# Performance work log

Hardware: AMD Instinct MI355X
Metric: run time of the kernel (lower is better)

The kernel has to match this reference:

```python
import jax, jax.numpy as jnp
import numpy as np

H = 8                                  # n_heads
MULS = [256, 128, 64]                  # multiplicities of attention_irreps * n_heads (l=0,1,2)
L_DIMS = [1, 3, 5]                     # 2l+1 for l = 0, 1, 2
NUM_IRREPS_PER_HEAD = sum(m // H for m in MULS)   # 32+16+8 = 56
ATTN_NORM = 1.0 / np.sqrt(NUM_IRREPS_PER_HEAD)


def _split(x):
    """Split flat irreps array [..., 960] into per-l blocks [..., mul, 2l+1]."""
    blocks, off = [], 0
    for m, d in zip(MULS, L_DIMS):
        blocks.append(x[..., off:off + m * d].reshape(x.shape[:-1] + (m, d)))
        off += m * d
    return blocks


def _e3_linear(blocks, Ws):
    # e3nn Linear: per-irrep channel mixing with 1/sqrt(fan_in) path normalization
    return [jnp.einsum('...mi,mn->...ni', b, W) / np.sqrt(b.shape[-2])
            for b, W in zip(blocks, Ws)]


def _mul_to_axis(blocks):
    # split multiplicity axis into [H, mul_per_head]
    return [b.reshape(b.shape[:-2] + (H, b.shape[-2] // H, b.shape[-1])) for b in blocks]


def _forward(x, wq0, wq1, wq2, wk0, wk1, wk2, wv0, wv1, wv2):
    xb = _split(x)
    q = _mul_to_axis(_e3_linear(xb, [wq0, wq1, wq2]))   # each [b, n, H, m, d]
    k = _mul_to_axis(_e3_linear(xb, [wk0, wk1, wk2]))
    v = _mul_to_axis(_e3_linear(xb, [wv0, wv1, wv2]))

    # elementwise tensor product filtered to 0e: per-irrep invariant dot / sqrt(2l+1),
    # then summed over all irrep channels (sum over axis=-1 in the original)
    logits = 0.0
    for qb, kb, d in zip(q, k, L_DIMS):
        logits = logits + jnp.einsum('bqhmd,bkhmd->bqkh', qb, kb) / np.sqrt(d)

    # softmax over the key-orbital axis (axis=-2 of [b, q, k, h])
    w = jax.nn.softmax(logits * ATTN_NORM, axis=2)

    # weighted sum over keys per irrep, then axis_to_mul(-2): merge head axis into mul
    outs = []
    for vb in v:
        u = jnp.einsum('bqkh,bkhmd->bqhmd', w, vb)      # [b, q, H, m, d]
        outs.append(u.reshape(u.shape[:2] + (-1,)))     # [b, q, H*m*d]
    update = jnp.concatenate(outs, axis=-1)             # [b, q, 960]

    return x + update  # residual: input irreps == update irreps


def setup_inputs() -> dict:
    key = jax.random.key(0)
    ks = jax.random.split(key, 10)
    B, N, D = 1024, 64, 960
    inp = {"x": jax.random.normal(ks[0], (B, N, D), dtype=jnp.float32)}
    names = ["wq0", "wq1", "wq2", "wk0", "wk1", "wk2", "wv0", "wv1", "wv2"]
    shapes = [(256, 256), (128, 128), (64, 64)] * 3
    for i, (nm, sh) in enumerate(zip(names, shapes)):
        inp[nm] = jax.random.normal(ks[i + 1], sh, dtype=jnp.float32)
    return inp


def reference(x, wq0, wq1, wq2, wk0, wk1, wk2, wv0, wv1, wv2):
    return _forward(x, wq0, wq1, wq2, wk0, wk1, wk2, wv0, wv1, wv2)
```

## Files before the change

### kernel.cpp

```cpp
#include <hip/hip_runtime.h>
#include <stdint.h>

typedef __attribute__((ext_vector_type(8))) short short8v;
typedef __attribute__((ext_vector_type(4))) float f32x4;

#define ATTN_NORM 0.13363062095621219f
#define LOG2E 1.4426950408889634f

__device__ __forceinline__ unsigned short f2bf(float f) {
  union { float f; uint32_t u; } v; v.f = f;
  uint32_t u = v.u;
  u += 0x7fffu + ((u >> 16) & 1u);
  return (unsigned short)(u >> 16);
}

__device__ __forceinline__ uint32_t pack2bf(float lo, float hi) {
  return (uint32_t)f2bf(lo) | ((uint32_t)f2bf(hi) << 16);
}

__global__ void prep_w2(const float* q0, const float* q1, const float* q2,
                        const float* k0, const float* k1, const float* k2,
                        const float* v0, const float* v1, const float* v2,
                        unsigned short* ws) {
  int e = blockIdx.x * 256 + threadIdx.x;
  if (e >= 258048) return;
  int b = e >> 9, idx = e & 511;
  int lane = idx >> 3, eo = idx & 7;
  int mat = b / 168, r = b - mat * 168;
  int li, n, MUL, c2, ks;
  if (r < 128) {
    li = 0; MUL = 256;
    int h = r >> 4, t = r & 15;
    int nt = t >> 3; c2 = (t >> 2) & 1; ks = t & 3;
    n = h * 32 + nt * 16 + (lane & 15);
  } else if (r < 160) {
    li = 1; MUL = 128;
    int r2 = r - 128; int h = r2 >> 2, t = r2 & 3;
    c2 = t >> 1; ks = t & 1;
    n = h * 16 + (lane & 15);
  } else {
    li = 2; MUL = 64;
    int r2 = r - 160; int hp = r2 >> 1;
    c2 = r2 & 1; ks = 0;
    n = hp * 16 + (lane & 15);
  }
  int m = c2 * (MUL >> 1) + ks * 32 + (lane >> 4) * 8 + eo;
  const float* src;
  if (mat == 0)      src = (li == 0) ? q0 : (li == 1) ? q1 : q2;
  else if (mat == 1) src = (li == 0) ? k0 : (li == 1) ? k1 : k2;
  else               src = (li == 0) ? v0 : (li == 1) ? v1 : v2;
  float scale = (li == 0) ? 0.0625f : (li == 1) ? 0.08838834764831845f : 0.125f;
  if (mat == 0) {
    float qext = (li == 0) ? 1.0f : (li == 1) ? 0.5773502691896258f : 0.4472135954999579f;
    scale *= ATTN_NORM * LOG2E * qext;
  }
  ws[e] = f2bf(src[m * MUL + n] * scale);
}

template<int W, int D, int XO, int BLK0, int NB>
__device__ __forceinline__ void conv_pass(const float* __restrict__ xp,
                                          unsigned short* __restrict__ xo,
                                          unsigned short* __restrict__ lds, int tid) {
  constexpr int PITCH = W + 8;
  #pragma unroll 2
  for (int f = tid; f < 64 * (W / 4); f += 256) {
    int tok = f / (W / 4);
    int c4 = f - tok * (W / 4);
    float4 v = *(const float4*)(xp + tok * 960 + XO + c4 * 4);
    uint2 pk = make_uint2(pack2bf(v.x, v.y), pack2bf(v.z, v.w));
    *(uint2*)(lds + tok * PITCH + c4 * 4) = pk;
  }
  __syncthreads();
  #pragma unroll 2
  for (int f = tid; f < NB * 64; f += 256) {
    int bl = f >> 6, lane = f & 63;
    int mb, i, qt;
    if (D == 1) {
      int c2 = bl >> 4, t = bl & 15;
      mb = c2 * 128 + (t >> 2) * 32; i = 0; qt = t & 3;
    } else if (D == 3) {
      int c2 = bl / 24; int t = bl - c2 * 24;
      int ks = t / 12; int rt = t - ks * 12;
      mb = c2 * 64 + ks * 32; i = rt >> 2; qt = rt & 3;
    } else {
      int c2 = bl / 20; int rt = bl - c2 * 20;
      mb = c2 * 32; i = rt >> 2; qt = rt & 3;
    }
    int tok = qt * 16 + (lane & 15);
    int m0 = mb + (lane >> 4) * 8;
    const unsigned short* base = lds + tok * PITCH + m0 * D + i;
    union { unsigned short o[8]; short8v s; } pk;
    #pragma unroll
    for (int e = 0; e < 8; ++e) pk.o[e] = base[e * D];
    *(short8v*)(xo + (BLK0 + bl) * 512 + lane * 8) = pk.s;
  }
}

__launch_bounds__(256)
__global__ void conv_x4(const float* __restrict__ x, unsigned short* __restrict__ xw) {
  __shared__ unsigned short lds[25088];
  int bid = blockIdx.x, tid = threadIdx.x;
  int b, pass;
  if (bid < 1024)       { b = bid;        pass = 0; }
  else if (bid < 2048)  { b = bid - 1024; pass = 1; }
  else                  { b = bid - 2048; pass = 2; }
  const float* xp = x + (size_t)b * 61440;
  unsigned short* xo = xw + (size_t)b * 61440;
  if (pass == 0)      conv_pass<256, 1,   0,  0, 32>(xp, xo, lds, tid);
  else if (pass == 1) conv_pass<384, 3, 256, 32, 48>(xp, xo, lds, tid);
  else                conv_pass<320, 5, 640, 80, 40>(xp, xo, lds, tid);
}

template<int L>
__device__ __forceinline__ void qkv_l(const unsigned short* __restrict__ xwb,
                                      const unsigned short* __restrict__ ws,
                                      char* __restrict__ sQ, char* __restrict__ sK,
                                      char* __restrict__ sVT,
                                      int h, int lane, int wvi) {
  constexpr int D    = (L == 0) ? 1 : (L == 1) ? 3 : 5;
  constexpr int NPL  = (L == 0) ? 32 : (L == 1) ? 16 : 8;
  constexpr int NT   = (L == 0) ? 2 : 1;
  constexpr int KS   = (L == 0) ? 4 : (L == 1) ? 2 : 1;
  constexpr int COFF = (L == 0) ? 0 : (L == 1) ? 32 : 80;
  constexpr int XB   = (L == 0) ? 0 : (L == 1) ? 32 : 80;
  constexpr int XC2  = KS * 4 * D;
  constexpr int NG   = 2 * KS;
  const int l15 = lane & 15, blk = lane >> 4;

  short8v xf[NG][D];
  #pragma unroll
  for (int g = 0; g < NG; ++g) {
    const int c2 = g / KS, ks = g - c2 * KS;
    #pragma unroll
    for (int j = 0; j < D; ++j)
      xf[g][j] = *(const short8v*)(xwb + (XB + c2 * XC2 + ks * 4 * D + j * 4 + wvi) * 512 + lane * 8);
  }

  f32x4 acc[3][NT][D];
  #pragma unroll
  for (int a = 0; a < 3; ++a)
    #pragma unroll
    for (int nt = 0; nt < NT; ++nt)
      #pragma unroll
      for (int j = 0; j < D; ++j)
        acc[a][nt][j] = (f32x4){0.f, 0.f, 0.f, 0.f};

  #pragma unroll
  for (int g = 0; g < NG; ++g) {
    const int c2 = g / KS, ks = g - c2 * KS;
    #pragma unroll
    for (int mat = 0; mat < 3; ++mat) {
      #pragma unroll
      for (int nt = 0; nt < NT; ++nt) {
        int wb;
        if constexpr (L == 0)      wb = mat * 168 + h * 16 + nt * 8 + c2 * 4 + ks;
        else if constexpr (L == 1) wb = mat * 168 + 128 + h * 4 + c2 * 2 + ks;
        else                       wb = mat * 168 + 160 + (h >> 1) * 2 + c2;
        short8v wf = *(const short8v*)(ws + wb * 512 + lane * 8);
        #pragma unroll
        for (int j = 0; j < D; ++j)
          acc[mat][nt][j] = __builtin_amdgcn_mfma_f32_16x16x32_bf16(wf, xf[g][j], acc[mat][nt][j], 0, 0, 0);
      }
    }
  }

  const int q = wvi * 16 + l15;
  const int qsw = (q & 7) << 4;
  #pragma unroll
  for (int nt = 0; nt < NT; ++nt) {
    #pragma unroll
    for (int j = 0; j < D; ++j) {
      int cb; bool valid;
      if constexpr (L == 2) { valid = ((blk >> 1) == (h & 1)); cb = COFF + j * NPL + (blk & 1) * 4; }
      else                  { valid = true;                    cb = COFF + j * NPL + nt * 16 + blk * 4; }
      if (valid) {
        uint32_t q01 = pack2bf(acc[0][nt][j][0], acc[0][nt][j][1]);
        uint32_t q23 = pack2bf(acc[0][nt][j][2], acc[0][nt][j][3]);
        uint32_t k01 = pack2bf(acc[1][nt][j][0], acc[1][nt][j][1]);
        uint32_t k23 = pack2bf(acc[1][nt][j][2], acc[1][nt][j][3]);
        int sw = (cb * 2) ^ qsw;
        *(uint2*)(sQ + q * 256 + sw) = make_uint2(q01, q23);
        *(uint2*)(sK + q * 256 + sw) = make_uint2(k01, k23);
        #pragma unroll
        for (int reg = 0; reg < 4; ++reg) {
          int c = cb + reg;
          *(unsigned short*)(sVT + c * 128 + ((q * 2) ^ ((c & 7) << 4))) = f2bf(acc[2][nt][j][reg]);
        }
      }
    }
  }
}

__launch_bounds__(256, 3)
__global__ void orbattn6(const float* __restrict__ x,
                         const unsigned short* __restrict__ ws,
                         const unsigned short* __restrict__ xw,
                         float* __restrict__ out) {
  extern __shared__ char smem[];
  char* sQ  = smem;
  char* sK  = smem + 16384;
  char* sVT = smem + 32768;
  char* sP  = smem;
  int tid = threadIdx.x;
  int bid = blockIdx.x;
  int xcd = bid & 7, t = bid >> 3;
  int h = t & 7;
  int b = (t >> 3) * 8 + xcd;
  const float* xb = x + (size_t)b * 61440;
  float* ob = out + (size_t)b * 61440;
  const unsigned short* xwb = xw + (size_t)b * 61440;
  const int lane = tid & 63, wvi = tid >> 6, l15 = lane & 15, blk = lane >> 4;

  for (int f = tid; f < 512; f += 256) {
    int q = f >> 3, c = 120 + (f & 7);
    int sw = (c * 2) ^ ((q & 7) << 4);
    *(unsigned short*)(sQ + q * 256 + sw) = 0;
    *(unsigned short*)(sK + q * 256 + sw) = 0;
    *(unsigned short*)(sVT + c * 128 + ((q * 2) ^ ((c & 7) << 4))) = 0;
  }

  qkv_l<0>(xwb, ws, sQ, sK, sVT, h, lane, wvi);
  qkv_l<1>(xwb, ws, sQ, sK, sVT, h, lane, wvi);
  qkv_l<2>(xwb, ws, sQ, sK, sVT, h, lane, wvi);
  __syncthreads();

  f32x4 lacc[4];
  #pragma unroll
  for (int kt = 0; kt < 4; ++kt) lacc[kt] = (f32x4){0.f, 0.f, 0.f, 0.f};
  #pragma unroll
  for (int ks = 0; ks < 4; ++ks) {
    int qr = wvi * 16 + l15;
    int bc = (ks * 32 + blk * 8) * 2;
    short8v qf = *(const short8v*)(sQ + qr * 256 + (bc ^ ((qr & 7) << 4)));
    #pragma unroll
    for (int kt = 0; kt < 4; ++kt) {
      int kr = kt * 16 + l15;
      short8v kf = *(const short8v*)(sK + kr * 256 + (bc ^ ((kr & 7) << 4)));
      lacc[kt] = __builtin_amdgcn_mfma_f32_16x16x32_bf16(qf, kf, lacc[kt], 0, 0, 0);
    }
  }
  float preg[4][4];
  #pragma unroll
  for (int reg = 0; reg < 4; ++reg) {
    float mx = fmaxf(fmaxf(lacc[0][reg], lacc[1][reg]), fmaxf(lacc[2][reg], lacc[3][reg]));
    #pragma unroll
    for (int dd = 1; dd <= 8; dd <<= 1) mx = fmaxf(mx, __shfl_xor(mx, dd, 64));
    float s = 0.f;
    #pragma unroll
    for (int kt = 0; kt < 4; ++kt) { preg[reg][kt] = exp2f(lacc[kt][reg] - mx); s += preg[reg][kt]; }
    #pragma unroll
    for (int dd = 1; dd <= 8; dd <<= 1) s += __shfl_xor(s, dd, 64);
    float inv = 1.0f / s;
    #pragma unroll
    for (int kt = 0; kt < 4; ++kt) preg[reg][kt] *= inv;
  }
  __syncthreads();

  #pragma unroll
  for (int reg = 0; reg < 4; ++reg) {
    int q = wvi * 16 + blk * 4 + reg;
    #pragma unroll
    for (int kt = 0; kt < 4; ++kt) {
      int k = kt * 16 + l15;
      *(unsigned short*)(sP + q * 128 + ((k * 2) ^ ((q & 7) << 4))) = f2bf(preg[reg][kt]);
    }
  }
  __syncthreads();

  f32x4 uacc[8];
  #pragma unroll
  for (int ct = 0; ct < 8; ++ct) uacc[ct] = (f32x4){0.f, 0.f, 0.f, 0.f};
  #pragma unroll
  for (int ks = 0; ks < 2; ++ks) {
    int qr = wvi * 16 + l15;
    int bc = (ks * 32 + blk * 8) * 2;
    short8v pf = *(const short8v*)(sP + qr * 128 + (bc ^ ((qr & 7) << 4)));
    #pragma unroll
    for (int ct = 0; ct < 8; ++ct) {
      int cr = ct * 16 + l15;
      short8v vf = *(const short8v*)(sVT + cr * 128 + (bc ^ ((cr & 7) << 4)));
      uacc[ct] = __builtin_amdgcn_mfma_f32_16x16x32_bf16(pf, vf, uacc[ct], 0, 0, 0);
    }
  }
  #pragma unroll
  for (int ct = 0; ct < 8; ++ct) {
    int c = ct * 16 + l15;
    if (c < 120) {
      int o;
      if (c < 32) o = h * 32 + c;
      else if (c < 80) { int cc = c - 32; int i = cc >> 4, nl = cc & 15; o = 256 + (h * 16 + nl) * 3 + i; }
      else             { int cc = c - 80; int i = cc >> 3, nl = cc & 7;  o = 640 + (h * 8 + nl) * 5 + i; }
      #pragma unroll
      for (int reg = 0; reg < 4; ++reg) {
        int q = wvi * 16 + blk * 4 + reg;
        int gi = q * 960 + o;
        ob[gi] = xb[gi] + uacc[ct][reg];
      }
    }
  }
}

extern "C" void kernel_launch(void* const* d_in, const int* in_sizes, int n_in,
                              void* d_out, int out_size, void* d_ws, size_t ws_size,
                              hipStream_t stream) {
  const float* x = (const float*)d_in[0];
  unsigned short* wsw = (unsigned short*)d_ws;
  unsigned short* xw = (unsigned short*)((char*)d_ws + 516096);
  float* out = (float*)d_out;
  prep_w2<<<1008, 256, 0, stream>>>(
      (const float*)d_in[1], (const float*)d_in[2], (const float*)d_in[3],
      (const float*)d_in[4], (const float*)d_in[5], (const float*)d_in[6],
      (const float*)d_in[7], (const float*)d_in[8], (const float*)d_in[9], wsw);
  conv_x4<<<3072, 256, 0, stream>>>(x, xw);
  hipFuncSetAttribute((const void*)orbattn6, hipFuncAttributeMaxDynamicSharedMemorySize, 49152);
  orbattn6<<<8192, 256, 49152, stream>>>(x, wsw, xw, out);
}
```

Measured before the change: 328.3 us.

## Defer V projection, reuse LDS regions, and stage output for vectorized residual stores

Splits the fused QKV projection so V is computed after softmax, writing V^T into the freed K region of LDS. This cuts shared memory from 48KB to 32KB and the live accumulators per phase, so occupancy can rise from 3 to 4 blocks per CU. The PV result is staged in LDS so the residual add and output write use contiguous float4 loads and stores instead of scattered scalar ones. In exchange the x tiles are reloaded for the V pass, and two extra barriers are added.

```diff
diff --git a/kernel.cpp b/kernel.cpp
--- a/kernel.cpp
+++ b/kernel.cpp
@@ -112,11 +112,10 @@
 }
 
 template<int L>
-__device__ __forceinline__ void qkv_l(const unsigned short* __restrict__ xwb,
-                                      const unsigned short* __restrict__ ws,
-                                      char* __restrict__ sQ, char* __restrict__ sK,
-                                      char* __restrict__ sVT,
-                                      int h, int lane, int wvi) {
+__device__ __forceinline__ void qk_l(const unsigned short* __restrict__ xwb,
+                                     const unsigned short* __restrict__ ws,
+                                     char* __restrict__ sQ, char* __restrict__ sK,
+                                     int h, int lane, int wvi) {
   constexpr int D    = (L == 0) ? 1 : (L == 1) ? 3 : 5;
   constexpr int NPL  = (L == 0) ? 32 : (L == 1) ? 16 : 8;
   constexpr int NT   = (L == 0) ? 2 : 1;
@@ -136,9 +135,9 @@
       xf[g][j] = *(const short8v*)(xwb + (XB + c2 * XC2 + ks * 4 * D + j * 4 + wvi) * 512 + lane * 8);
   }
 
-  f32x4 acc[3][NT][D];
-  #pragma unroll
-  for (int a = 0; a < 3; ++a)
+  f32x4 acc[2][NT][D];
+  #pragma unroll
+  for (int a = 0; a < 2; ++a)
     #pragma unroll
     for (int nt = 0; nt < NT; ++nt)
       #pragma unroll
@@ -149,7 +148,7 @@
   for (int g = 0; g < NG; ++g) {
     const int c2 = g / KS, ks = g - c2 * KS;
     #pragma unroll
-    for (int mat = 0; mat < 3; ++mat) {
+    for (int mat = 0; mat < 2; ++mat) {
       #pragma unroll
       for (int nt = 0; nt < NT; ++nt) {
         int wb;
@@ -181,26 +180,88 @@
         int sw = (cb * 2) ^ qsw;
         *(uint2*)(sQ + q * 256 + sw) = make_uint2(q01, q23);
         *(uint2*)(sK + q * 256 + sw) = make_uint2(k01, k23);
+      }
+    }
+  }
+}
+
+template<int L>
+__device__ __forceinline__ void v_l(const unsigned short* __restrict__ xwb,
+                                    const unsigned short* __restrict__ ws,
+                                    char* __restrict__ sVT,
+                                    int h, int lane, int wvi) {
+  constexpr int D    = (L == 0) ? 1 : (L == 1) ? 3 : 5;
+  constexpr int NPL  = (L == 0) ? 32 : (L == 1) ? 16 : 8;
+  constexpr int NT   = (L == 0) ? 2 : 1;
+  constexpr int KS   = (L == 0) ? 4 : (L == 1) ? 2 : 1;
+  constexpr int COFF = (L == 0) ? 0 : (L == 1) ? 32 : 80;
+  constexpr int XB   = (L == 0) ? 0 : (L == 1) ? 32 : 80;
+  constexpr int XC2  = KS * 4 * D;
+  constexpr int NG   = 2 * KS;
+  const int l15 = lane & 15, blk = lane >> 4;
+
+  short8v xf[NG][D];
+  #pragma unroll
+  for (int g = 0; g < NG; ++g) {
+    const int c2 = g / KS, ks = g - c2 * KS;
+    #pragma unroll
+    for (int j = 0; j < D; ++j)
+      xf[g][j] = *(const short8v*)(xwb + (XB + c2 * XC2 + ks * 4 * D + j * 4 + wvi) * 512 + lane * 8);
+  }
+
+  f32x4 acc[NT][D];
+  #pragma unroll
+  for (int nt = 0; nt < NT; ++nt)
+    #pragma unroll
+    for (int j = 0; j < D; ++j)
+      acc[nt][j] = (f32x4){0.f, 0.f, 0.f, 0.f};
+
+  #pragma unroll
+  for (int g = 0; g < NG; ++g) {
+    const int c2 = g / KS, ks = g - c2 * KS;
+    #pragma unroll
+    for (int nt = 0; nt < NT; ++nt) {
+      int wb;
+      if constexpr (L == 0)      wb = 2 * 168 + h * 16 + nt * 8 + c2 * 4 + ks;
+      else if constexpr (L == 1) wb = 2 * 168 + 128 + h * 4 + c2 * 2 + ks;
+      else                       wb = 2 * 168 + 160 + (h >> 1) * 2 + c2;
+      short8v wf = *(const short8v*)(ws + wb * 512 + lane * 8);
+      #pragma unroll
+      for (int j = 0; j < D; ++j)
+        acc[nt][j] = __builtin_amdgcn_mfma_f32_16x16x32_bf16(wf, xf[g][j], acc[nt][j], 0, 0, 0);
+    }
+  }
+
+  const int q = wvi * 16 + l15;
+  #pragma unroll
+  for (int nt = 0; nt < NT; ++nt) {
+    #pragma unroll
+    for (int j = 0; j < D; ++j) {
+      int cb; bool valid;
+      if constexpr (L == 2) { valid = ((blk >> 1) == (h & 1)); cb = COFF + j * NPL + (blk & 1) * 4; }
+      else                  { valid = true;                    cb = COFF + j * NPL + nt * 16 + blk * 4; }
+      if (valid) {
         #pragma unroll
         for (int reg = 0; reg < 4; ++reg) {
           int c = cb + reg;
-          *(unsigned short*)(sVT + c * 128 + ((q * 2) ^ ((c & 7) << 4))) = f2bf(acc[2][nt][j][reg]);
+          *(unsigned short*)(sVT + c * 128 + ((q * 2) ^ ((c & 7) << 4))) = f2bf(acc[nt][j][reg]);
         }
       }
     }
   }
 }
 
-__launch_bounds__(256, 3)
-__global__ void orbattn6(const float* __restrict__ x,
+__launch_bounds__(256, 4)
+__global__ void orbattn7(const float* __restrict__ x,
                          const unsigned short* __restrict__ ws,
                          const unsigned short* __restrict__ xw,
                          float* __restrict__ out) {
   extern __shared__ char smem[];
   char* sQ  = smem;
   char* sK  = smem + 16384;
-  char* sVT = smem + 32768;
   char* sP  = smem;
+  char* sVT = smem + 16384;
+  float* sU = (float*)smem;
   int tid = threadIdx.x;
   int bid = blockIdx.x;
   int xcd = bid & 7, t = bid >> 3;
@@ -216,12 +277,11 @@
     int sw = (c * 2) ^ ((q & 7) << 4);
     *(unsigned short*)(sQ + q * 256 + sw) = 0;
     *(unsigned short*)(sK + q * 256 + sw) = 0;
-    *(unsigned short*)(sVT + c * 128 + ((q * 2) ^ ((c & 7) << 4))) = 0;
-  }
-
-  qkv_l<0>(xwb, ws, sQ, sK, sVT, h, lane, wvi);
-  qkv_l<1>(xwb, ws, sQ, sK, sVT, h, lane, wvi);
-  qkv_l<2>(xwb, ws, sQ, sK, sVT, h, lane, wvi);
+  }
+
+  qk_l<0>(xwb, ws, sQ, sK, h, lane, wvi);
+  qk_l<1>(xwb, ws, sQ, sK, h, lane, wvi);
+  qk_l<2>(xwb, ws, sQ, sK, h, lane, wvi);
   __syncthreads();
 
   f32x4 lacc[4];
@@ -265,6 +325,13 @@
       *(unsigned short*)(sP + q * 128 + ((k * 2) ^ ((q & 7) << 4))) = f2bf(preg[reg][kt]);
     }
   }
+  for (int f = tid; f < 512; f += 256) {
+    int q = f & 63, c = 120 + (f >> 6);
+    *(unsigned short*)(sVT + c * 128 + ((q * 2) ^ ((c & 7) << 4))) = 0;
+  }
+  v_l<0>(xwb, ws, sVT, h, lane, wvi);
+  v_l<1>(xwb, ws, sVT, h, lane, wvi);
+  v_l<2>(xwb, ws, sVT, h, lane, wvi);
   __syncthreads();
 
   f32x4 uacc[8];
@@ -282,21 +349,34 @@
       uacc[ct] = __builtin_amdgcn_mfma_f32_16x16x32_bf16(pf, vf, uacc[ct], 0, 0, 0);
     }
   }
+  __syncthreads();
+
   #pragma unroll
   for (int ct = 0; ct < 8; ++ct) {
     int c = ct * 16 + l15;
     if (c < 120) {
-      int o;
-      if (c < 32) o = h * 32 + c;
-      else if (c < 80) { int cc = c - 32; int i = cc >> 4, nl = cc & 15; o = 256 + (h * 16 + nl) * 3 + i; }
-      else             { int cc = c - 80; int i = cc >> 3, nl = cc & 7;  o = 640 + (h * 8 + nl) * 5 + i; }
+      int col;
+      if (c < 32) col = c;
+      else if (c < 80) { int cc = c - 32; col = 32 + (cc & 15) * 3 + (cc >> 4); }
+      else             { int cc = c - 80; col = 80 + (cc & 7) * 5 + (cc >> 3); }
       #pragma unroll
       for (int reg = 0; reg < 4; ++reg) {
-        int q = wvi * 16 + blk * 4 + reg;
-        int gi = q * 960 + o;
-        ob[gi] = xb[gi] + uacc[ct][reg];
+        int tok = wvi * 16 + blk * 4 + reg;
+        sU[tok * 124 + col] = uacc[ct][reg];
       }
     }
+  }
+  __syncthreads();
+
+  const int hb0 = h * 32, hb1 = 256 + h * 48, hb2 = 640 + h * 40;
+  for (int f = tid; f < 1920; f += 256) {
+    int tok = f / 30;
+    int s4 = (f - tok * 30) * 4;
+    int o = (s4 < 32) ? (hb0 + s4) : (s4 < 80) ? (hb1 + s4 - 32) : (hb2 + s4 - 80);
+    f32x4 u = *(const f32x4*)(sU + tok * 124 + s4);
+    f32x4 xv = *(const f32x4*)(xb + tok * 960 + o);
+    f32x4 r = u + xv;
+    *(f32x4*)(ob + tok * 960 + o) = r;
   }
 }
 
@@ -312,6 +392,6 @@
       (const float*)d_in[4], (const float*)d_in[5], (const float*)d_in[6],
       (const float*)d_in[7], (const float*)d_in[8], (const float*)d_in[9], wsw);
   conv_x4<<<3072, 256, 0, stream>>>(x, xw);
-  hipFuncSetAttribute((const void*)orbattn6, hipFuncAttributeMaxDynamicSharedMemorySize, 49152);
-  orbattn6<<<8192, 256, 49152, stream>>>(x, wsw, xw, out);
-}
+  hipFuncSetAttribute((const void*)orbattn7, hipFuncAttributeMaxDynamicSharedMemorySize, 32768);
+  orbattn7<<<8192, 256, 32768, stream>>>(x, wsw, xw, out);
+}
```

Result: slower. 374.9 us (+14.2%).

## Keep V projection in registers and alias V^T over K buffer to cut LDS

Applied to the files above, without the earlier changes.

The V projection accumulators now stay in registers (10 f32x4 per lane) through the logits and softmax phases and are written to LDS only after K is no longer needed, so V^T reuses the K region. This cuts dynamic shared memory from 48KB to 32KB per block, and launch bounds go from 3 to 4 blocks per CU to raise occupancy. The cost is 40 extra live VGPRs across the softmax phase, which under the tighter register budget could cause spills.

```diff
diff --git a/kernel.cpp b/kernel.cpp
--- a/kernel.cpp
+++ b/kernel.cpp
@@ -115,7 +115,7 @@
 __device__ __forceinline__ void qkv_l(const unsigned short* __restrict__ xwb,
                                       const unsigned short* __restrict__ ws,
                                       char* __restrict__ sQ, char* __restrict__ sK,
-                                      char* __restrict__ sVT,
+                                      f32x4* __restrict__ vacc,
                                       int h, int lane, int wvi) {
   constexpr int D    = (L == 0) ? 1 : (L == 1) ? 3 : 5;
   constexpr int NPL  = (L == 0) ? 32 : (L == 1) ? 16 : 8;
@@ -125,6 +125,7 @@
   constexpr int XB   = (L == 0) ? 0 : (L == 1) ? 32 : 80;
   constexpr int XC2  = KS * 4 * D;
   constexpr int NG   = 2 * KS;
+  constexpr int VOFF = (L == 0) ? 0 : (L == 1) ? 2 : 5;
   const int l15 = lane & 15, blk = lane >> 4;
 
   short8v xf[NG][D];
@@ -136,9 +137,9 @@
       xf[g][j] = *(const short8v*)(xwb + (XB + c2 * XC2 + ks * 4 * D + j * 4 + wvi) * 512 + lane * 8);
   }
 
-  f32x4 acc[3][NT][D];
-  #pragma unroll
-  for (int a = 0; a < 3; ++a)
+  f32x4 acc[2][NT][D];
+  #pragma unroll
+  for (int a = 0; a < 2; ++a)
     #pragma unroll
     for (int nt = 0; nt < NT; ++nt)
       #pragma unroll
@@ -149,7 +150,7 @@
   for (int g = 0; g < NG; ++g) {
     const int c2 = g / KS, ks = g - c2 * KS;
     #pragma unroll
-    for (int mat = 0; mat < 3; ++mat) {
+    for (int mat = 0; mat < 2; ++mat) {
       #pragma unroll
       for (int nt = 0; nt < NT; ++nt) {
         int wb;
@@ -161,6 +162,17 @@
         for (int j = 0; j < D; ++j)
           acc[mat][nt][j] = __builtin_amdgcn_mfma_f32_16x16x32_bf16(wf, xf[g][j], acc[mat][nt][j], 0, 0, 0);
       }
+    }
+    #pragma unroll
+    for (int nt = 0; nt < NT; ++nt) {
+      int wb;
+      if constexpr (L == 0)      wb = 2 * 168 + h * 16 + nt * 8 + c2 * 4 + ks;
+      else if constexpr (L == 1) wb = 2 * 168 + 128 + h * 4 + c2 * 2 + ks;
+      else                       wb = 2 * 168 + 160 + (h >> 1) * 2 + c2;
+      short8v wf = *(const short8v*)(ws + wb * 512 + lane * 8);
+      #pragma unroll
+      for (int j = 0; j < D; ++j)
+        vacc[VOFF + nt * D + j] = __builtin_amdgcn_mfma_f32_16x16x32_bf16(wf, xf[g][j], vacc[VOFF + nt * D + j], 0, 0, 0);
     }
   }
 
@@ -181,26 +193,50 @@
         int sw = (cb * 2) ^ qsw;
         *(uint2*)(sQ + q * 256 + sw) = make_uint2(q01, q23);
         *(uint2*)(sK + q * 256 + sw) = make_uint2(k01, k23);
+      }
+    }
+  }
+}
+
+template<int L>
+__device__ __forceinline__ void vwrite_l(char* __restrict__ sVT,
+                                         const f32x4* __restrict__ vacc,
+                                         int h, int lane, int wvi) {
+  constexpr int D    = (L == 0) ? 1 : (L == 1) ? 3 : 5;
+  constexpr int NPL  = (L == 0) ? 32 : (L == 1) ? 16 : 8;
+  constexpr int NT   = (L == 0) ? 2 : 1;
+  constexpr int COFF = (L == 0) ? 0 : (L == 1) ? 32 : 80;
+  constexpr int VOFF = (L == 0) ? 0 : (L == 1) ? 2 : 5;
+  const int l15 = lane & 15, blk = lane >> 4;
+  const int q = wvi * 16 + l15;
+  #pragma unroll
+  for (int nt = 0; nt < NT; ++nt) {
+    #pragma unroll
+    for (int j = 0; j < D; ++j) {
+      int cb; bool valid;
+      if constexpr (L == 2) { valid = ((blk >> 1) == (h & 1)); cb = COFF + j * NPL + (blk & 1) * 4; }
+      else                  { valid = true;                    cb = COFF + j * NPL + nt * 16 + blk * 4; }
+      if (valid) {
         #pragma unroll
         for (int reg = 0; reg < 4; ++reg) {
           int c = cb + reg;
-          *(unsigned short*)(sVT + c * 128 + ((q * 2) ^ ((c & 7) << 4))) = f2bf(acc[2][nt][j][reg]);
+          *(unsigned short*)(sVT + c * 128 + ((q * 2) ^ ((c & 7) << 4))) = f2bf(vacc[VOFF + nt * D + j][reg]);
         }
       }
     }
   }
 }
 
-__launch_bounds__(256, 3)
-__global__ void orbattn6(const float* __restrict__ x,
-                         const unsigned short* __restrict__ ws,
-                         const unsigned short* __restrict__ xw,
-                         float* __restrict__ out) {
+__launch_bounds__(256, 4)
+__global__ void orbattn11(const float* __restrict__ x,
+                          const unsigned short* __restrict__ ws,
+                          const unsigned short* __restrict__ xw,
+                          float* __restrict__ out) {
   extern __shared__ char smem[];
   char* sQ  = smem;
   char* sK  = smem + 16384;
-  char* sVT = smem + 32768;
   char* sP  = smem;
+  char* sVT = smem + 16384;
   int tid = threadIdx.x;
   int bid = blockIdx.x;
   int xcd = bid & 7, t = bid >> 3;
@@ -216,12 +252,15 @@
     int sw = (c * 2) ^ ((q & 7) << 4);
     *(unsigned short*)(sQ + q * 256 + sw) = 0;
     *(unsigned short*)(sK + q * 256 + sw) = 0;
-    *(unsigned short*)(sVT + c * 128 + ((q * 2) ^ ((c & 7) << 4))) = 0;
-  }
-
-  qkv_l<0>(xwb, ws, sQ, sK, sVT, h, lane, wvi);
-  qkv_l<1>(xwb, ws, sQ, sK, sVT, h, lane, wvi);
-  qkv_l<2>(xwb, ws, sQ, sK, sVT, h, lane, wvi);
+  }
+
+  f32x4 vacc[10];
+  #pragma unroll
+  for (int i = 0; i < 10; ++i) vacc[i] = (f32x4){0.f, 0.f, 0.f, 0.f};
+
+  qkv_l<0>(xwb, ws, sQ, sK, vacc, h, lane, wvi);
+  qkv_l<1>(xwb, ws, sQ, sK, vacc, h, lane, wvi);
+  qkv_l<2>(xwb, ws, sQ, sK, vacc, h, lane, wvi);
   __syncthreads();
 
   f32x4 lacc[4];
@@ -265,6 +304,13 @@
       *(unsigned short*)(sP + q * 128 + ((k * 2) ^ ((q & 7) << 4))) = f2bf(preg[reg][kt]);
     }
   }
+  for (int f = tid; f < 512; f += 256) {
+    int q = f & 63, c = 120 + (f >> 6);
+    *(unsigned short*)(sVT + c * 128 + ((q * 2) ^ ((c & 7) << 4))) = 0;
+  }
+  vwrite_l<0>(sVT, vacc, h, lane, wvi);
+  vwrite_l<1>(sVT, vacc, h, lane, wvi);
+  vwrite_l<2>(sVT, vacc, h, lane, wvi);
   __syncthreads();
 
   f32x4 uacc[8];
@@ -312,6 +358,6 @@
       (const float*)d_in[4], (const float*)d_in[5], (const float*)d_in[6],
       (const float*)d_in[7], (const float*)d_in[8], (const float*)d_in[9], wsw);
   conv_x4<<<3072, 256, 0, stream>>>(x, xw);
-  hipFuncSetAttribute((const void*)orbattn6, hipFuncAttributeMaxDynamicSharedMemorySize, 49152);
-  orbattn6<<<8192, 256, 49152, stream>>>(x, wsw, xw, out);
-}
+  hipFuncSetAttribute((const void*)orbattn11, hipFuncAttributeMaxDynamicSharedMemorySize, 32768);
+  orbattn11<<<8192, 256, 32768, stream>>>(x, wsw, xw, out);
+}
```

After: 371.4 us. 1.13x slower.
